# Performance work log

Measured on AMD Instinct MI355X. Metric: run time of the kernel, lower is better.

The kernel has to match this reference:

```python
import jax, jax.numpy as jnp
import numpy as np
import math

H = 4            # cross_attn_heads
SPARSE_RATIO = 0.6
B, N, C = 128, 196, 768


def setup_inputs() -> dict:
    key = jax.random.key(0)
    ks = jax.random.split(key, 10)
    xav = (6.0 / (C + C)) ** 0.5  # xavier_uniform bound for square Linear
    inp = {
        "RGB_cash": jax.random.normal(ks[0], (B, N, C), jnp.float32),
        "NI_cash": jax.random.normal(ks[1], (B, N, C), jnp.float32),
        "TI_cash": jax.random.normal(ks[2], (B, N, C), jnp.float32),
        "RGB_global": jax.random.normal(ks[3], (B, C), jnp.float32),
        "NI_global": jax.random.normal(ks[4], (B, C), jnp.float32),
        "TI_global": jax.random.normal(ks[5], (B, C), jnp.float32),
        # 9 CrossModalAttention modules, stacked: q_proj / k_proj weights (out,in) and biases
        "q_w": jax.random.uniform(ks[6], (9, C, C), jnp.float32, -xav, xav),
        "q_b": jnp.zeros((9, C), jnp.float32),
        "k_w": jax.random.uniform(ks[7], (9, C, C), jnp.float32, -xav, xav),
        "k_b": jnp.zeros((9, C), jnp.float32),
        # 3 TokenSparse modal_weights, init torch.ones(3); small noise for non-degenerate softmax
        "modal_w": jnp.ones((3, 3), jnp.float32) + 0.01 * jax.random.normal(ks[8], (3, 3), jnp.float32),
    }
    return inp


def _cos_sim(patches, g):
    # patches (B,N,C), g (B,C) -> (B,N); F.normalize eps=1e-12
    pn = patches / jnp.maximum(jnp.linalg.norm(patches, axis=-1, keepdims=True), 1e-12)
    gn = g / jnp.maximum(jnp.linalg.norm(g, axis=-1, keepdims=True), 1e-12)
    return jnp.einsum("bnc,bc->bn", pn, gn)


def _cross_attn(patches, g, cos, qw, qb, kw, kb):
    # CrossModalAttention.forward: Q from global (1 token), K from patches, softmax over N
    b, n, c = patches.shape
    d = c // H
    q = (g @ qw.T + qb).reshape(b, H, d)              # (B,H,D)
    k = (patches @ kw.T + kb).reshape(b, n, H, d)     # (B,N,H,D)
    attn = jnp.einsum("bhd,bnhd->bhn", q, k) * (d ** -0.5)
    attn = jax.nn.softmax(attn, axis=-1)              # (B,H,N)
    return (attn * cos[:, None, :]).mean(axis=1)      # (B,N)


def _minmax(s):
    smin = s.min(axis=-1, keepdims=True)
    smax = s.max(axis=-1, keepdims=True)
    return (s - smin) / (smax - smin + 1e-8)


def _token_sparse(tokens, s_im, s_m2, s_m3, mw):
    b, n, c = tokens.shape
    w = jax.nn.softmax(mw)
    score = w[0] * _minmax(s_im) + w[1] * _minmax(s_m2) + w[2] * _minmax(s_m3)
    num_keep = max(1, math.ceil(n * SPARSE_RATIO))
    _, idx = jax.lax.top_k(score, num_keep)           # == descending sort, first num_keep
    mask = jnp.zeros((b, n), score.dtype).at[jnp.arange(b)[:, None], idx].set(1.0)
    return tokens * mask[..., None], mask


def reference(RGB_cash, NI_cash, TI_cash, RGB_global, NI_global, TI_global,
              q_w, q_b, k_w, k_b, modal_w):
    toks = [RGB_cash, NI_cash, TI_cash]
    glbs = [RGB_global, NI_global, TI_global]
    # module order: rgb_self, rgb_x_nir, rgb_x_tir, nir_self, nir_x_rgb, nir_x_tir,
    #               tir_self, tir_x_rgb, tir_x_nir
    order = [(0, 0), (0, 1), (0, 2), (1, 1), (1, 0), (1, 2), (2, 2), (2, 0), (2, 1)]
    scores = []
    for i, (pi, gi) in enumerate(order):
        cos = _cos_sim(toks[pi], glbs[gi])
        scores.append(_cross_attn(toks[pi], glbs[gi], cos, q_w[i], q_b[i], k_w[i], k_b[i]))
    out_rgb, m_rgb = _token_sparse(RGB_cash, scores[0], scores[1], scores[2], modal_w[0])
    out_nir, m_nir = _token_sparse(NI_cash, scores[3], scores[4], scores[5], modal_w[1])
    out_tir, m_tir = _token_sparse(TI_cash, scores[6], scores[7], scores[8], modal_w[2])
    return (out_rgb, out_nir, out_tir, m_rgb, m_nir, m_tir)
```

## Files before the change

### kernel.cpp

```cpp
#include <hip/hip_runtime.h>
#include <math.h>

#define BB   128
#define NN   196
#define CC   768
#define HH   4
#define DD   192
#define TOK_PER   19267584
#define NROWS_ALL 75264
#define F4_ALL    14450688
#define NUM_KEEP  118
#define SCALE_D   0.07216878364870322f

#define OFF_QPART 0
#define SZ_QPART  (2*9*128*768)
#define OFF_VV    (OFF_QPART + SZ_QPART)
#define SZ_VV     (9*128*4*768)
#define OFF_BIAS  (OFF_VV + SZ_VV)
#define SZ_BIAS   (9*128*4)
#define OFF_GN    (OFF_BIAS + SZ_BIAS)
#define SZ_GN     (3*128*768)
#define OFF_SC    (OFF_GN + SZ_GN)
#define SZ_SC     (3*128*196*16)

__device__ __forceinline__ float4 f4fma(float s, float4 b, float4 a) {
  a.x = fmaf(s, b.x, a.x); a.y = fmaf(s, b.y, a.y);
  a.z = fmaf(s, b.z, a.z); a.w = fmaf(s, b.w, a.w);
  return a;
}
__device__ __forceinline__ float f4dot(float4 p, float4 q) {
  return p.x*q.x + p.y*q.y + p.z*q.z + p.w*q.w;
}

__global__ __launch_bounds__(256) void k_gnorm(const float* __restrict__ g0,
                                               const float* __restrict__ g1,
                                               const float* __restrict__ g2,
                                               float* __restrict__ gn) {
  int wid = (blockIdx.x * 256 + threadIdx.x) >> 6;
  int lane = threadIdx.x & 63;
  if (wid >= 384) return;
  int t = wid >> 7, b = wid & 127;
  const float* src = (t == 0) ? g0 : ((t == 1) ? g1 : g2);
  const float4* s4 = (const float4*)(src + (size_t)b * CC);
  float4 v0 = s4[lane], v1 = s4[lane + 64], v2 = s4[lane + 128];
  float ss = f4dot(v0,v0) + f4dot(v1,v1) + f4dot(v2,v2);
  #pragma unroll
  for (int off = 32; off; off >>= 1) ss += __shfl_xor(ss, off);
  float inv = 1.0f / fmaxf(sqrtf(ss), 1e-12f);
  float4* d4 = (float4*)(gn + ((size_t)t * 128 + b) * CC);
  v0.x *= inv; v0.y *= inv; v0.z *= inv; v0.w *= inv;
  v1.x *= inv; v1.y *= inv; v1.z *= inv; v1.w *= inv;
  v2.x *= inv; v2.y *= inv; v2.z *= inv; v2.w *= inv;
  d4[lane] = v0; d4[lane + 64] = v1; d4[lane + 128] = v2;
}

__global__ __launch_bounds__(256) void k_qproj(const float* __restrict__ g0,
                                               const float* __restrict__ g1,
                                               const float* __restrict__ g2,
                                               const float* __restrict__ qw,
                                               float* __restrict__ qpart) {
  __shared__ __align__(16) float AsT[32 * 68];
  __shared__ __align__(16) float WsT[32 * 68];
  const int gtab[9] = {0, 1, 2, 1, 0, 2, 2, 0, 1};
  int i = blockIdx.y, z = blockIdx.z;
  int mt = blockIdx.x & 1, nt = blockIdx.x >> 1;
  int tid = threadIdx.x, tx = tid & 15, ty = tid >> 4;
  int gi = gtab[i];
  const float4* A4 = (const float4*)((gi == 0) ? g0 : ((gi == 1) ? g1 : g2));
  const float4* W4 = (const float4*)(qw + (size_t)i * CC * CC);
  float4 acc0 = {0,0,0,0}, acc1 = {0,0,0,0}, acc2 = {0,0,0,0}, acc3 = {0,0,0,0};
  int arow = mt * 64, wrow = nt * 64;
  int kb4 = z * 96;
  for (int kk = 0; kk < 12; kk++) {
    #pragma unroll
    for (int f = tid; f < 512; f += 256) {
      int r = f >> 3, k4 = f & 7;
      float4 va = A4[(size_t)(arow + r) * 192 + kb4 + kk * 8 + k4];
      float4 vw = W4[(size_t)(wrow + r) * 192 + kb4 + kk * 8 + k4];
      int kq = 4 * k4;
      AsT[(kq+0)*68 + r] = va.x; AsT[(kq+1)*68 + r] = va.y;
      AsT[(kq+2)*68 + r] = va.z; AsT[(kq+3)*68 + r] = va.w;
      WsT[(kq+0)*68 + r] = vw.x; WsT[(kq+1)*68 + r] = vw.y;
      WsT[(kq+2)*68 + r] = vw.z; WsT[(kq+3)*68 + r] = vw.w;
    }
    __syncthreads();
    #pragma unroll
    for (int k = 0; k < 32; k++) {
      float4 a = *(const float4*)&AsT[k * 68 + 4 * ty];
      float4 w = *(const float4*)&WsT[k * 68 + 4 * tx];
      acc0 = f4fma(a.x, w, acc0); acc1 = f4fma(a.y, w, acc1);
      acc2 = f4fma(a.z, w, acc2); acc3 = f4fma(a.w, w, acc3);
    }
    __syncthreads();
  }
  float* dst = qpart + (size_t)(z * 9 + i) * 128 * CC;
  int col = wrow + 4 * tx;
  int row = arow + 4 * ty;
  *(float4*)&dst[(size_t)(row + 0) * CC + col] = acc0;
  *(float4*)&dst[(size_t)(row + 1) * CC + col] = acc1;
  *(float4*)&dst[(size_t)(row + 2) * CC + col] = acc2;
  *(float4*)&dst[(size_t)(row + 3) * CC + col] = acc3;
}

__global__ __launch_bounds__(256) void k_vvproj(const float* __restrict__ qpart,
                                                const float* __restrict__ qb,
                                                const float* __restrict__ kw,
                                                float* __restrict__ vvout) {
  __shared__ __align__(16) float AsT[32 * 68];
  __shared__ __align__(16) float Bs[32 * 68];
  int ih = blockIdx.y; int i = ih >> 2, h = ih & 3;
  int mt = blockIdx.x & 1, nt = blockIdx.x >> 1;
  int tid = threadIdx.x, tx = tid & 15, ty = tid >> 4;
  const float4* qp0 = (const float4*)qpart + (size_t)i * 128 * 192;
  const float4* qp1 = (const float4*)qpart + (size_t)(9 + i) * 128 * 192;
  const float4* qb4 = (const float4*)qb + (size_t)i * 192;
  const float4* B4  = (const float4*)(kw + (size_t)i * CC * CC);
  float4 acc0 = {0,0,0,0}, acc1 = {0,0,0,0}, acc2 = {0,0,0,0}, acc3 = {0,0,0,0};
  int arow = mt * 64;
  int bcol4 = nt * 16;
  for (int kk = 0; kk < 6; kk++) {
    #pragma unroll
    for (int f = tid; f < 512; f += 256) {
      int r = f >> 3, k4 = f & 7;
      int colf4 = h * 48 + kk * 8 + k4;
      float4 va = qp0[(size_t)(arow + r) * 192 + colf4];
      float4 vb = qp1[(size_t)(arow + r) * 192 + colf4];
      float4 vq = qb4[colf4];
      va.x += vb.x + vq.x; va.y += vb.y + vq.y;
      va.z += vb.z + vq.z; va.w += vb.w + vq.w;
      int kq = 4 * k4;
      AsT[(kq+0)*68 + r] = va.x; AsT[(kq+1)*68 + r] = va.y;
      AsT[(kq+2)*68 + r] = va.z; AsT[(kq+3)*68 + r] = va.w;
      int rk = f >> 4, c4 = f & 15;
      float4 vB = B4[(size_t)(h * DD + kk * 32 + rk) * 192 + bcol4 + c4];
      *(float4*)&Bs[rk * 68 + 4 * c4] = vB;
    }
    __syncthreads();
    #pragma unroll
    for (int k = 0; k < 32; k++) {
      float4 a = *(const float4*)&AsT[k * 68 + 4 * ty];
      float4 bb = *(const float4*)&Bs[k * 68 + 4 * tx];
      acc0 = f4fma(a.x, bb, acc0); acc1 = f4fma(a.y, bb, acc1);
      acc2 = f4fma(a.z, bb, acc2); acc3 = f4fma(a.w, bb, acc3);
    }
    __syncthreads();
  }
  int col = nt * 64 + 4 * tx;
  int b0 = arow + 4 * ty;
  *(float4*)&vvout[((size_t)(i * 128 + b0 + 0) * 4 + h) * CC + col] = acc0;
  *(float4*)&vvout[((size_t)(i * 128 + b0 + 1) * 4 + h) * CC + col] = acc1;
  *(float4*)&vvout[((size_t)(i * 128 + b0 + 2) * 4 + h) * CC + col] = acc2;
  *(float4*)&vvout[((size_t)(i * 128 + b0 + 3) * 4 + h) * CC + col] = acc3;
}

__global__ __launch_bounds__(128) void k_bias(const float* __restrict__ qpart,
                                              const float* __restrict__ qb,
                                              const float* __restrict__ kb,
                                              float* __restrict__ bias) {
  int ih = blockIdx.x; int i = ih >> 2, h = ih & 3;
  int b = threadIdx.x;
  const float* q0  = qpart + ((size_t)i * 128 + b) * CC + h * DD;
  const float* q1  = qpart + ((size_t)(9 + i) * 128 + b) * CC + h * DD;
  const float* qbb = qb + (size_t)i * CC + h * DD;
  const float* kbb = kb + (size_t)i * CC + h * DD;
  float s = 0.f;
  for (int j = 0; j < DD; j++) s = fmaf(q0[j] + q1[j] + qbb[j], kbb[j], s);
  bias[((size_t)i * 128 + b) * 4 + h] = s;
}

__global__ __launch_bounds__(256, 2) void k_dots2(const float* __restrict__ rgb,
                                                  const float* __restrict__ ni,
                                                  const float* __restrict__ ti,
                                                  const float* __restrict__ vv,
                                                  const float* __restrict__ gn,
                                                  const float* __restrict__ bias,
                                                  float* __restrict__ sc) {
  __shared__ float red[4][64 * 17];
  int bid = blockIdx.x;
  int t = bid >> 8;
  int rem = bid & 255;
  int b = rem >> 1, half = rem & 1;
  int tid = threadIdx.x;
  int w = tid >> 6, lane = tid & 63;
  const float* toks = (t == 0) ? rgb : ((t == 1) ? ni : ti);
  int gi0, gi1, gi2;
  if (t == 0)      { gi0 = 0; gi1 = 1; gi2 = 2; }
  else if (t == 1) { gi0 = 1; gi1 = 0; gi2 = 2; }
  else             { gi0 = 2; gi1 = 0; gi2 = 1; }

  float4 V[45];
  #pragma unroll
  for (int k = 0; k < 3; k++) {
    #pragma unroll
    for (int h = 0; h < 4; h++) {
      const float4* src = (const float4*)(vv + (((size_t)(3*t + k) * 128 + b) * 4 + h) * CC);
      int v = k * 4 + h;
      V[3*v + 0] = src[lane];
      V[3*v + 1] = src[lane + 64];
      V[3*v + 2] = src[lane + 128];
    }
  }
  {
    int gidx0 = gi0, gidx1 = gi1, gidx2 = gi2;
    const float4* s0 = (const float4*)(gn + ((size_t)gidx0 * 128 + b) * CC);
    const float4* s1 = (const float4*)(gn + ((size_t)gidx1 * 128 + b) * CC);
    const float4* s2 = (const float4*)(gn + ((size_t)gidx2 * 128 + b) * CC);
    V[36] = s0[lane]; V[37] = s0[lane + 64]; V[38] = s0[lane + 128];
    V[39] = s1[lane]; V[40] = s1[lane + 64]; V[41] = s1[lane + 128];
    V[42] = s2[lane]; V[43] = s2[lane + 64]; V[44] = s2[lane + 128];
  }

  int a_id = lane & 15;
  float bias_r = 0.f;
  if (a_id < 12)
    bias_r = bias[((size_t)(3*t + (a_id >> 2)) * 128 + b) * 4 + (a_id & 3)];

  float* myred = red[w];
  int s_grp = lane >> 4;
  int n0 = half * 98;

  const float4* pr0 = (const float4*)(toks + ((size_t)b * NN + n0 + w) * CC);
  float4 pc0 = pr0[lane], pc1 = pr0[lane + 64], pc2 = pr0[lane + 128];

  for (int it = 0; it < 25; it++) {
    int row_local = it * 4 + w;
    if (row_local >= 98) break;

    float a[16];
    #pragma unroll
    for (int v = 0; v < 15; v++) {
      a[v] = f4dot(pc0, V[3*v]) + f4dot(pc1, V[3*v + 1]) + f4dot(pc2, V[3*v + 2]);
    }
    a[15] = f4dot(pc0, pc0) + f4dot(pc1, pc1) + f4dot(pc2, pc2);

    int rl_next = row_local + 4;
    float4 pn0, pn1, pn2;
    if (rl_next < 98) {
      const float4* pr = (const float4*)(toks + ((size_t)b * NN + n0 + rl_next) * CC);
      pn0 = pr[lane]; pn1 = pr[lane + 64]; pn2 = pr[lane + 128];
    }

    #pragma unroll
    for (int v = 0; v < 16; v++) myred[lane * 17 + v] = a[v];
    __builtin_amdgcn_s_waitcnt(0);
    float part = 0.f;
    #pragma unroll
    for (int i = 0; i < 16; i++)
      part += myred[(s_grp * 16 + i) * 17 + a_id];
    part += __shfl_xor(part, 16, 64);
    part += __shfl_xor(part, 32, 64);

    float s15  = __shfl(part, 15, 64);
    float invp = 1.0f / fmaxf(sqrtf(s15), 1e-12f);
    float res;
    if (a_id < 12)      res = (part + bias_r) * SCALE_D;
    else if (a_id < 15) res = part * invp;
    else                res = invp;

    if (lane < 16) {
      float* scrow = sc + (((size_t)t * 128 + b) * 196 + (n0 + row_local)) * 16;
      scrow[lane] = res;
    }
    pc0 = pn0; pc1 = pn1; pc2 = pn2;
  }
}

__device__ __forceinline__ float bred_sum(float v, float* red) {
  #pragma unroll
  for (int off = 32; off; off >>= 1) v += __shfl_xor(v, off);
  int tid = threadIdx.x;
  if ((tid & 63) == 0) red[tid >> 6] = v;
  __syncthreads();
  v = (red[0] + red[1]) + (red[2] + red[3]);
  __syncthreads();
  return v;
}
__device__ __forceinline__ float bred_max(float v, float* red) {
  #pragma unroll
  for (int off = 32; off; off >>= 1) v = fmaxf(v, __shfl_xor(v, off));
  int tid = threadIdx.x;
  if ((tid & 63) == 0) red[tid >> 6] = v;
  __syncthreads();
  v = fmaxf(fmaxf(red[0], red[1]), fmaxf(red[2], red[3]));
  __syncthreads();
  return v;
}
__device__ __forceinline__ float bred_min(float v, float* red) {
  #pragma unroll
  for (int off = 32; off; off >>= 1) v = fminf(v, __shfl_xor(v, off));
  int tid = threadIdx.x;
  if ((tid & 63) == 0) red[tid >> 6] = v;
  __syncthreads();
  v = fminf(fminf(red[0], red[1]), fminf(red[2], red[3]));
  __syncthreads();
  return v;
}

__global__ __launch_bounds__(256) void k_score(const float* __restrict__ sc,
                                               const float* __restrict__ modal_w,
                                               float* __restrict__ outmask) {
  __shared__ float red[4];
  __shared__ float sfinal[196];
  int b = blockIdx.x, m = blockIdx.y;
  int tid = threadIdx.x;
  bool act = tid < NN;
  const float* row = sc + (((size_t)m * 128 + b) * 196 + (act ? tid : 0)) * 16;
  float w0 = modal_w[m * 3 + 0], w1 = modal_w[m * 3 + 1], w2 = modal_w[m * 3 + 2];
  float wm = fmaxf(w0, fmaxf(w1, w2));
  float e0 = expf(w0 - wm), e1 = expf(w1 - wm), e2 = expf(w2 - wm);
  float esum = e0 + e1 + e2;
  float wk[3] = {e0 / esum, e1 / esum, e2 / esum};
  float finalv = 0.f;
  for (int k = 0; k < 3; k++) {
    float asum = 0.f;
    for (int h = 0; h < 4; h++) {
      float v = act ? row[k * 4 + h] : -3.4e38f;
      float mx = bred_max(v, red);
      float e = act ? expf(v - mx) : 0.f;
      float s = bred_sum(e, red);
      asum += e / s;
    }
    float c = act ? row[12 + k] : 0.f;
    float scv = c * asum * 0.25f;
    float mn = bred_min(act ? scv : 3.4e38f, red);
    float mx = bred_max(act ? scv : -3.4e38f, red);
    finalv += wk[k] * (scv - mn) / (mx - mn + 1e-8f);
  }
  if (act) sfinal[tid] = finalv;
  __syncthreads();
  if (act) {
    int cnt = 0;
    for (int j = 0; j < NN; j++) {
      float fj = sfinal[j];
      cnt += (fj > finalv) || (fj == finalv && j < tid);
    }
    outmask[((size_t)m * 128 + b) * NN + tid] = (cnt < NUM_KEEP) ? 1.0f : 0.0f;
  }
}

__global__ __launch_bounds__(256) void k_write(const float* __restrict__ rgb,
                                               const float* __restrict__ ni,
                                               const float* __restrict__ ti,
                                               const float* __restrict__ maskbuf,
                                               float* __restrict__ out) {
  int idx = blockIdx.x * 256 + threadIdx.x;
  int r = idx / 192;
  int c4 = idx - r * 192;
  int m = r / 25088;
  int rb = r - m * 25088;
  float mv = maskbuf[r];
  const float* src = (m == 0) ? rgb : ((m == 1) ? ni : ti);
  float4 o = {0.f, 0.f, 0.f, 0.f};
  if (mv != 0.0f) o = ((const float4*)src)[(size_t)rb * 192 + c4];
  ((float4*)out)[idx] = o;
}

extern "C" void kernel_launch(void* const* d_in, const int* in_sizes, int n_in,
                              void* d_out, int out_size, void* d_ws, size_t ws_size,
                              hipStream_t stream) {
  const float* rgb = (const float*)d_in[0];
  const float* ni  = (const float*)d_in[1];
  const float* ti  = (const float*)d_in[2];
  const float* g0  = (const float*)d_in[3];
  const float* g1  = (const float*)d_in[4];
  const float* g2  = (const float*)d_in[5];
  const float* qw  = (const float*)d_in[6];
  const float* qb  = (const float*)d_in[7];
  const float* kw  = (const float*)d_in[8];
  const float* kb  = (const float*)d_in[9];
  const float* mw  = (const float*)d_in[10];

  float* ws    = (float*)d_ws;
  float* qpart = ws + OFF_QPART;
  float* vv    = ws + OFF_VV;
  float* bias  = ws + OFF_BIAS;
  float* gn    = ws + OFF_GN;
  float* sc    = ws + OFF_SC;
  float* outf  = (float*)d_out;
  float* maskb = outf + (size_t)3 * TOK_PER;

  k_gnorm<<<96, 256, 0, stream>>>(g0, g1, g2, gn);
  k_qproj<<<dim3(24, 9, 2), 256, 0, stream>>>(g0, g1, g2, qw, qpart);
  k_vvproj<<<dim3(24, 36), 256, 0, stream>>>(qpart, qb, kw, vv);
  k_bias<<<36, 128, 0, stream>>>(qpart, qb, kb, bias);
  k_dots2<<<768, 256, 0, stream>>>(rgb, ni, ti, vv, gn, bias, sc);
  k_score<<<dim3(128, 3), 256, 0, stream>>>(sc, mw, maskb);
  k_write<<<F4_ALL / 256, 256, 0, stream>>>(rgb, ni, ti, maskb, outf);
}
```

Before: 565.1 us.

## Fuse global normalization into dots kernel, parallelize bias and score reductions

```diff
diff --git a/kernel.cpp b/kernel.cpp
--- a/kernel.cpp
+++ b/kernel.cpp
@@ -30,28 +30,6 @@
 }
 __device__ __forceinline__ float f4dot(float4 p, float4 q) {
   return p.x*q.x + p.y*q.y + p.z*q.z + p.w*q.w;
-}
-
-__global__ __launch_bounds__(256) void k_gnorm(const float* __restrict__ g0,
-                                               const float* __restrict__ g1,
-                                               const float* __restrict__ g2,
-                                               float* __restrict__ gn) {
-  int wid = (blockIdx.x * 256 + threadIdx.x) >> 6;
-  int lane = threadIdx.x & 63;
-  if (wid >= 384) return;
-  int t = wid >> 7, b = wid & 127;
-  const float* src = (t == 0) ? g0 : ((t == 1) ? g1 : g2);
-  const float4* s4 = (const float4*)(src + (size_t)b * CC);
-  float4 v0 = s4[lane], v1 = s4[lane + 64], v2 = s4[lane + 128];
-  float ss = f4dot(v0,v0) + f4dot(v1,v1) + f4dot(v2,v2);
-  #pragma unroll
-  for (int off = 32; off; off >>= 1) ss += __shfl_xor(ss, off);
-  float inv = 1.0f / fmaxf(sqrtf(ss), 1e-12f);
-  float4* d4 = (float4*)(gn + ((size_t)t * 128 + b) * CC);
-  v0.x *= inv; v0.y *= inv; v0.z *= inv; v0.w *= inv;
-  v1.x *= inv; v1.y *= inv; v1.z *= inv; v1.w *= inv;
-  v2.x *= inv; v2.y *= inv; v2.z *= inv; v2.w *= inv;
-  d4[lane] = v0; d4[lane + 64] = v1; d4[lane + 128] = v2;
 }
 
 __global__ __launch_bounds__(256) void k_qproj(const float* __restrict__ g0,
@@ -153,29 +131,41 @@
   *(float4*)&vvout[((size_t)(i * 128 + b0 + 3) * 4 + h) * CC + col] = acc3;
 }
 
-__global__ __launch_bounds__(128) void k_bias(const float* __restrict__ qpart,
+__global__ __launch_bounds__(256) void k_bias(const float* __restrict__ qpart,
                                               const float* __restrict__ qb,
                                               const float* __restrict__ kb,
                                               float* __restrict__ bias) {
   int ih = blockIdx.x; int i = ih >> 2, h = ih & 3;
-  int b = threadIdx.x;
-  const float* q0  = qpart + ((size_t)i * 128 + b) * CC + h * DD;
-  const float* q1  = qpart + ((size_t)(9 + i) * 128 + b) * CC + h * DD;
+  int w = threadIdx.x >> 6, lane = threadIdx.x & 63;
   const float* qbb = qb + (size_t)i * CC + h * DD;
   const float* kbb = kb + (size_t)i * CC + h * DD;
-  float s = 0.f;
-  for (int j = 0; j < DD; j++) s = fmaf(q0[j] + q1[j] + qbb[j], kbb[j], s);
-  bias[((size_t)i * 128 + b) * 4 + h] = s;
+  float kb0 = kbb[lane], kb1 = kbb[lane + 64], kb2 = kbb[lane + 128];
+  float qb0 = qbb[lane], qb1 = qbb[lane + 64], qb2 = qbb[lane + 128];
+  const float* q0base = qpart + (size_t)i * 128 * CC + h * DD;
+  const float* q1base = qpart + (size_t)(9 + i) * 128 * CC + h * DD;
+  for (int b = w; b < 128; b += 4) {
+    const float* q0 = q0base + (size_t)b * CC;
+    const float* q1 = q1base + (size_t)b * CC;
+    float s = (q0[lane]       + q1[lane]       + qb0) * kb0
+            + (q0[lane + 64]  + q1[lane + 64]  + qb1) * kb1
+            + (q0[lane + 128] + q1[lane + 128] + qb2) * kb2;
+    #pragma unroll
+    for (int off = 32; off; off >>= 1) s += __shfl_xor(s, off);
+    if (lane == 0) bias[((size_t)i * 128 + b) * 4 + h] = s;
+  }
 }
 
 __global__ __launch_bounds__(256, 2) void k_dots2(const float* __restrict__ rgb,
                                                   const float* __restrict__ ni,
                                                   const float* __restrict__ ti,
                                                   const float* __restrict__ vv,
-                                                  const float* __restrict__ gn,
+                                                  const float* __restrict__ g0,
+                                                  const float* __restrict__ g1,
+                                                  const float* __restrict__ g2,
                                                   const float* __restrict__ bias,
                                                   float* __restrict__ sc) {
   __shared__ float red[4][64 * 17];
+  __shared__ __align__(16) float GN[3 * CC];
   int bid = blockIdx.x;
   int t = bid >> 8;
   int rem = bid & 255;
@@ -188,7 +178,23 @@
   else if (t == 1) { gi0 = 1; gi1 = 0; gi2 = 2; }
   else             { gi0 = 2; gi1 = 0; gi2 = 1; }
 
-  float4 V[45];
+  if (w < 3) {
+    int gidx = (w == 0) ? gi0 : ((w == 1) ? gi1 : gi2);
+    const float* gsrc = (gidx == 0) ? g0 : ((gidx == 1) ? g1 : g2);
+    const float4* s4 = (const float4*)(gsrc + (size_t)b * CC);
+    float4 u0 = s4[lane], u1 = s4[lane + 64], u2 = s4[lane + 128];
+    float ss = f4dot(u0, u0) + f4dot(u1, u1) + f4dot(u2, u2);
+    #pragma unroll
+    for (int off = 32; off; off >>= 1) ss += __shfl_xor(ss, off);
+    float inv = 1.0f / fmaxf(sqrtf(ss), 1e-12f);
+    u0.x *= inv; u0.y *= inv; u0.z *= inv; u0.w *= inv;
+    u1.x *= inv; u1.y *= inv; u1.z *= inv; u1.w *= inv;
+    u2.x *= inv; u2.y *= inv; u2.z *= inv; u2.w *= inv;
+    float4* d4 = (float4*)&GN[w * CC];
+    d4[lane] = u0; d4[lane + 64] = u1; d4[lane + 128] = u2;
+  }
+
+  float4 V[36];
   #pragma unroll
   for (int k = 0; k < 3; k++) {
     #pragma unroll
@@ -200,22 +206,16 @@
       V[3*v + 2] = src[lane + 128];
     }
   }
-  {
-    int gidx0 = gi0, gidx1 = gi1, gidx2 = gi2;
-    const float4* s0 = (const float4*)(gn + ((size_t)gidx0 * 128 + b) * CC);
-    const float4* s1 = (const float4*)(gn + ((size_t)gidx1 * 128 + b) * CC);
-    const float4* s2 = (const float4*)(gn + ((size_t)gidx2 * 128 + b) * CC);
-    V[36] = s0[lane]; V[37] = s0[lane + 64]; V[38] = s0[lane + 128];
-    V[39] = s1[lane]; V[40] = s1[lane + 64]; V[41] = s1[lane + 128];
-    V[42] = s2[lane]; V[43] = s2[lane + 64]; V[44] = s2[lane + 128];
-  }
 
   int a_id = lane & 15;
   float bias_r = 0.f;
   if (a_id < 12)
     bias_r = bias[((size_t)(3*t + (a_id >> 2)) * 128 + b) * 4 + (a_id & 3)];
 
+  __syncthreads();
+
   float* myred = red[w];
+  const float4* G4 = (const float4*)GN;
   int s_grp = lane >> 4;
   int n0 = half * 98;
 
@@ -226,27 +226,32 @@
     int row_local = it * 4 + w;
     if (row_local >= 98) break;
 
-    float a[16];
-    #pragma unroll
-    for (int v = 0; v < 15; v++) {
-      a[v] = f4dot(pc0, V[3*v]) + f4dot(pc1, V[3*v + 1]) + f4dot(pc2, V[3*v + 2]);
-    }
-    a[15] = f4dot(pc0, pc0) + f4dot(pc1, pc1) + f4dot(pc2, pc2);
-
     int rl_next = row_local + 4;
-    float4 pn0, pn1, pn2;
+    float4 pn0 = pc0, pn1 = pc1, pn2 = pc2;
     if (rl_next < 98) {
       const float4* pr = (const float4*)(toks + ((size_t)b * NN + n0 + rl_next) * CC);
       pn0 = pr[lane]; pn1 = pr[lane + 64]; pn2 = pr[lane + 128];
     }
 
+    float a[16];
+    #pragma unroll
+    for (int v = 0; v < 12; v++)
+      a[v] = f4dot(pc0, V[3*v]) + f4dot(pc1, V[3*v + 1]) + f4dot(pc2, V[3*v + 2]);
+    #pragma unroll
+    for (int j = 0; j < 3; j++)
+      a[12 + j] = f4dot(pc0, G4[j*192 + lane])
+                + f4dot(pc1, G4[j*192 + lane + 64])
+                + f4dot(pc2, G4[j*192 + lane + 128]);
+    a[15] = f4dot(pc0, pc0) + f4dot(pc1, pc1) + f4dot(pc2, pc2);
+
     #pragma unroll
     for (int v = 0; v < 16; v++) myred[lane * 17 + v] = a[v];
-    __builtin_amdgcn_s_waitcnt(0);
+    __builtin_amdgcn_s_waitcnt(0xc07f);
+    __builtin_amdgcn_sched_barrier(0);
     float part = 0.f;
     #pragma unroll
-    for (int i = 0; i < 16; i++)
-      part += myred[(s_grp * 16 + i) * 17 + a_id];
+    for (int i2 = 0; i2 < 16; i2++)
+      part += myred[(s_grp * 16 + i2) * 17 + a_id];
     part += __shfl_xor(part, 16, 64);
     part += __shfl_xor(part, 32, 64);
 
@@ -265,74 +270,101 @@
   }
 }
 
-__device__ __forceinline__ float bred_sum(float v, float* red) {
-  #pragma unroll
-  for (int off = 32; off; off >>= 1) v += __shfl_xor(v, off);
-  int tid = threadIdx.x;
-  if ((tid & 63) == 0) red[tid >> 6] = v;
-  __syncthreads();
-  v = (red[0] + red[1]) + (red[2] + red[3]);
-  __syncthreads();
-  return v;
-}
-__device__ __forceinline__ float bred_max(float v, float* red) {
-  #pragma unroll
-  for (int off = 32; off; off >>= 1) v = fmaxf(v, __shfl_xor(v, off));
-  int tid = threadIdx.x;
-  if ((tid & 63) == 0) red[tid >> 6] = v;
-  __syncthreads();
-  v = fmaxf(fmaxf(red[0], red[1]), fmaxf(red[2], red[3]));
-  __syncthreads();
-  return v;
-}
-__device__ __forceinline__ float bred_min(float v, float* red) {
-  #pragma unroll
-  for (int off = 32; off; off >>= 1) v = fminf(v, __shfl_xor(v, off));
-  int tid = threadIdx.x;
-  if ((tid & 63) == 0) red[tid >> 6] = v;
-  __syncthreads();
-  v = fminf(fminf(red[0], red[1]), fminf(red[2], red[3]));
-  __syncthreads();
-  return v;
-}
-
 __global__ __launch_bounds__(256) void k_score(const float* __restrict__ sc,
                                                const float* __restrict__ modal_w,
                                                float* __restrict__ outmask) {
-  __shared__ float red[4];
+  __shared__ float S[196 * 17];
+  __shared__ float CSUM[12];
+  __shared__ float SV[3][196];
+  __shared__ float MN[3], MX[3];
   __shared__ float sfinal[196];
   int b = blockIdx.x, m = blockIdx.y;
   int tid = threadIdx.x;
+  int w = tid >> 6, lane = tid & 63;
   bool act = tid < NN;
-  const float* row = sc + (((size_t)m * 128 + b) * 196 + (act ? tid : 0)) * 16;
+
+  const float4* base = (const float4*)(sc + ((size_t)m * 128 + b) * 196 * 16);
+  if (act) {
+    float4 r0 = base[tid*4+0], r1 = base[tid*4+1], r2 = base[tid*4+2], r3 = base[tid*4+3];
+    float* d = &S[tid * 17];
+    d[0] = r0.x; d[1] = r0.y; d[2]  = r0.z; d[3]  = r0.w;
+    d[4] = r1.x; d[5] = r1.y; d[6]  = r1.z; d[7]  = r1.w;
+    d[8] = r2.x; d[9] = r2.y; d[10] = r2.z; d[11] = r2.w;
+    d[12] = r3.x; d[13] = r3.y; d[14] = r3.z;
+  }
+  __syncthreads();
+
+  #pragma unroll
+  for (int c = w; c < 12; c += 4) {
+    int n3 = lane + 192;
+    float v0 = S[(lane      ) * 17 + c];
+    float v1 = S[(lane +  64) * 17 + c];
+    float v2 = S[(lane + 128) * 17 + c];
+    float v3 = (n3 < NN) ? S[n3 * 17 + c] : -3.4e38f;
+    float mx = fmaxf(fmaxf(v0, v1), fmaxf(v2, v3));
+    #pragma unroll
+    for (int off = 32; off; off >>= 1) mx = fmaxf(mx, __shfl_xor(mx, off));
+    float e0 = expf(v0 - mx), e1 = expf(v1 - mx), e2 = expf(v2 - mx);
+    float e3 = (n3 < NN) ? expf(v3 - mx) : 0.f;
+    float es = e0 + e1 + e2 + e3;
+    #pragma unroll
+    for (int off = 32; off; off >>= 1) es += __shfl_xor(es, off);
+    S[(lane      ) * 17 + c] = e0;
+    S[(lane +  64) * 17 + c] = e1;
+    S[(lane + 128) * 17 + c] = e2;
+    if (n3 < NN) S[n3 * 17 + c] = e3;
+    if (lane == 0) CSUM[c] = es;
+  }
+  __syncthreads();
+
+  float scv0 = 0.f, scv1 = 0.f, scv2 = 0.f;
+  if (act) {
+    const float* r = &S[tid * 17];
+    float as0 = r[0]/CSUM[0] + r[1]/CSUM[1] + r[2]/CSUM[2]  + r[3]/CSUM[3];
+    float as1 = r[4]/CSUM[4] + r[5]/CSUM[5] + r[6]/CSUM[6]  + r[7]/CSUM[7];
+    float as2 = r[8]/CSUM[8] + r[9]/CSUM[9] + r[10]/CSUM[10] + r[11]/CSUM[11];
+    scv0 = r[12] * as0 * 0.25f;
+    scv1 = r[13] * as1 * 0.25f;
+    scv2 = r[14] * as2 * 0.25f;
+    SV[0][tid] = scv0; SV[1][tid] = scv1; SV[2][tid] = scv2;
+  }
+  __syncthreads();
+
+  if (w < 3) {
+    float u0 = SV[w][lane], u1 = SV[w][lane + 64], u2 = SV[w][lane + 128];
+    float mn = fminf(fminf(u0, u1), u2);
+    float mx = fmaxf(fmaxf(u0, u1), u2);
+    if (lane + 192 < NN) {
+      float u3 = SV[w][lane + 192];
+      mn = fminf(mn, u3); mx = fmaxf(mx, u3);
+    }
+    #pragma unroll
+    for (int off = 32; off; off >>= 1) {
+      mn = fminf(mn, __shfl_xor(mn, off));
+      mx = fmaxf(mx, __shfl_xor(mx, off));
+    }
+    if (lane == 0) { MN[w] = mn; MX[w] = mx; }
+  }
+  __syncthreads();
+
   float w0 = modal_w[m * 3 + 0], w1 = modal_w[m * 3 + 1], w2 = modal_w[m * 3 + 2];
   float wm = fmaxf(w0, fmaxf(w1, w2));
-  float e0 = expf(w0 - wm), e1 = expf(w1 - wm), e2 = expf(w2 - wm);
-  float esum = e0 + e1 + e2;
-  float wk[3] = {e0 / esum, e1 / esum, e2 / esum};
-  float finalv = 0.f;
-  for (int k = 0; k < 3; k++) {
-    float asum = 0.f;
-    for (int h = 0; h < 4; h++) {
-      float v = act ? row[k * 4 + h] : -3.4e38f;
-      float mx = bred_max(v, red);
-      float e = act ? expf(v - mx) : 0.f;
-      float s = bred_sum(e, red);
-      asum += e / s;
-    }
-    float c = act ? row[12 + k] : 0.f;
-    float scv = c * asum * 0.25f;
-    float mn = bred_min(act ? scv : 3.4e38f, red);
-    float mx = bred_max(act ? scv : -3.4e38f, red);
-    finalv += wk[k] * (scv - mn) / (mx - mn + 1e-8f);
-  }
-  if (act) sfinal[tid] = finalv;
-  __syncthreads();
+  float ew0 = expf(w0 - wm), ew1 = expf(w1 - wm), ew2 = expf(w2 - wm);
+  float esum = ew0 + ew1 + ew2;
+  float fv = 0.f;
+  if (act) {
+    fv = (ew0 / esum) * (scv0 - MN[0]) / (MX[0] - MN[0] + 1e-8f)
+       + (ew1 / esum) * (scv1 - MN[1]) / (MX[1] - MN[1] + 1e-8f)
+       + (ew2 / esum) * (scv2 - MN[2]) / (MX[2] - MN[2] + 1e-8f);
+    sfinal[tid] = fv;
+  }
+  __syncthreads();
+
   if (act) {
     int cnt = 0;
     for (int j = 0; j < NN; j++) {
       float fj = sfinal[j];
-      cnt += (fj > finalv) || (fj == finalv && j < tid);
+      cnt += (fj > fv) || (fj == fv && j < tid);
     }
     outmask[((size_t)m * 128 + b) * NN + tid] = (cnt < NUM_KEEP) ? 1.0f : 0.0f;
   }
@@ -374,16 +406,14 @@
   float* qpart = ws + OFF_QPART;
   float* vv    = ws + OFF_VV;
   float* bias  = ws + OFF_BIAS;
-  float* gn    = ws + OFF_GN;
   float* sc    = ws + OFF_SC;
   float* outf  = (float*)d_out;
   float* maskb = outf + (size_t)3 * TOK_PER;
 
-  k_gnorm<<<96, 256, 0, stream>>>(g0, g1, g2, gn);
   k_qproj<<<dim3(24, 9, 2), 256, 0, stream>>>(g0, g1, g2, qw, qpart);
   k_vvproj<<<dim3(24, 36), 256, 0, stream>>>(qpart, qb, kw, vv);
-  k_bias<<<36, 128, 0, stream>>>(qpart, qb, kb, bias);
-  k_dots2<<<768, 256, 0, stream>>>(rgb, ni, ti, vv, gn, bias, sc);
+  k_bias<<<36, 256, 0, stream>>>(qpart, qb, kb, bias);
+  k_dots2<<<768, 256, 0, stream>>>(rgb, ni, ti, vv, g0, g1, g2, bias, sc);
   k_score<<<dim3(128, 3), 256, 0, stream>>>(sc, mw, maskb);
   k_write<<<F4_ALL / 256, 256, 0, stream>>>(rgb, ni, ti, maskb, outf);
 }
```

Measured after the change: 556.0 us. Within noise of the previous version (-1.6%).
